# Optimization experiments

Measured on AMD Instinct MI355X. Metric: run time of the kernel, lower is better.

The kernel has to match this reference:

```python
import jax, jax.numpy as jnp
import numpy as np

N, E = 40000, 640000
IN, HID, OUT = 128, 128, 128


def _lin(key, fan_in, fan_out):
    bound = 1.0 / np.sqrt(fan_in)
    kw, kb = jax.random.split(key)
    W = jax.random.uniform(kw, (fan_in, fan_out), jnp.float32, -bound, bound)
    b = jax.random.uniform(kb, (fan_out,), jnp.float32, -bound, bound)
    return W, b


def setup_inputs() -> dict:
    key = jax.random.key(0)
    ks = jax.random.split(key, 10)
    node_feat = jax.random.normal(ks[0], (N, IN), jnp.float32)
    coord_feat = jax.random.normal(ks[1], (N, 3), jnp.float32)
    src = jax.random.randint(ks[2], (E,), 0, N, jnp.int32)
    dst = jax.random.randint(ks[3], (E,), 0, N, jnp.int32)
    # edge_mlp: Linear(2*IN+1 -> HID), SiLU, Linear(HID -> HID), SiLU
    We1, be1 = _lin(ks[4], 2 * IN + 1, HID)
    We2, be2 = _lin(ks[5], HID, HID)
    # node_mlp: Linear(IN+HID -> HID), SiLU, Linear(HID -> OUT)
    Wn1, bn1 = _lin(ks[6], IN + HID, HID)
    Wn2, bn2 = _lin(ks[7], HID, OUT)
    # coord_mlp: Linear(HID -> HID), SiLU, Linear(HID -> 1, bias=False)
    Wc1, bc1 = _lin(ks[8], HID, HID)
    Wc2, _ = _lin(ks[9], HID, 1)
    return {"node_feat": node_feat, "coord_feat": coord_feat, "src": src, "dst": dst,
            "We1": We1, "be1": be1, "We2": We2, "be2": be2,
            "Wn1": Wn1, "bn1": bn1, "Wn2": Wn2, "bn2": bn2,
            "Wc1": Wc1, "bc1": bc1, "Wc2": Wc2}


def reference(node_feat, coord_feat, src, dst,
              We1, be1, We2, be2, Wn1, bn1, Wn2, bn2, Wc1, bc1, Wc2):
    n = node_feat.shape[0]
    # edge gather: u_sub_v gives x_src - x_dst
    x_diff = coord_feat[src] - coord_feat[dst]                       # (E, 3)
    dist = jnp.sqrt(jnp.sum(x_diff * x_diff, axis=-1, keepdims=True))  # (E, 1)
    x_dir = x_diff / (dist + 1e-7)
    f = jnp.concatenate([node_feat[src], node_feat[dst], dist], axis=-1)  # (E, 2*IN+1)
    msg_h = jax.nn.silu(jax.nn.silu(f @ We1 + be1) @ We2 + be2)      # (E, HID)
    coef = jax.nn.silu(msg_h @ Wc1 + bc1) @ Wc2                      # (E, 1)
    msg_x = coef * x_dir                                             # (E, 3)
    # scatter-reduce to destination nodes: sum for h, mean for x
    h_neigh = jax.ops.segment_sum(msg_h, dst, num_segments=n)        # (N, HID)
    cnt = jax.ops.segment_sum(jnp.ones((dst.shape[0], 1), msg_x.dtype), dst, num_segments=n)
    x_neigh = jax.ops.segment_sum(msg_x, dst, num_segments=n) / jnp.maximum(cnt, 1.0)
    h = jax.nn.silu(jnp.concatenate([node_feat, h_neigh], axis=-1) @ Wn1 + bn1) @ Wn2 + bn2
    return h, coord_feat + x_neigh
```

## Files before the change

kernel.cpp:

```cpp
#include <hip/hip_runtime.h>
#include <hip/hip_bf16.h>
#include <math.h>
#include <stdint.h>

#define N_NODES 40000
#define N_EDGES 640000

typedef short short8 __attribute__((ext_vector_type(8)));
typedef float f32x4 __attribute__((ext_vector_type(4)));

__device__ __forceinline__ float silu(float x) {
    return __fdividef(x, 1.0f + __expf(-x));
}

__device__ __forceinline__ unsigned short f2bf(float f) {
    unsigned u = __float_as_uint(f);
    u += 0x7FFF + ((u >> 16) & 1);
    return (unsigned short)(u >> 16);
}
__device__ __forceinline__ float bf2f(unsigned short h) {
    return __uint_as_float(((unsigned)h) << 16);
}
__device__ __forceinline__ unsigned pk2bf(float a, float b) {
    __hip_bfloat162 h = __float22bfloat162_rn(make_float2(a, b));
    unsigned u;
    __builtin_memcpy(&u, &h, 4);
    return u;
}

__global__ __launch_bounds__(1024) void k_scan(const int* __restrict__ deg,
                                               int* __restrict__ row_start) {
    __shared__ int wsum[16];
    const int t = threadIdx.x;
    const int lane = t & 63, wid = t >> 6;
    int base = 0;
    if (t == 0) row_start[0] = 0;
    for (int off = 0; off < N_NODES; off += 1024) {
        int x = (off + t < N_NODES) ? deg[off + t] : 0;
#pragma unroll
        for (int s = 1; s < 64; s <<= 1) {
            const int u = __shfl_up(x, s, 64);
            if (lane >= s) x += u;
        }
        if (lane == 63) wsum[wid] = x;
        __syncthreads();
        if (wid == 0) {
            int ws = (lane < 16) ? wsum[lane] : 0;
#pragma unroll
            for (int s = 1; s < 16; s <<= 1) {
                const int u = __shfl_up(ws, s, 64);
                if (lane >= s) ws += u;
            }
            if (lane < 16) wsum[lane] = ws;
        }
        __syncthreads();
        const int wbase = (wid > 0) ? wsum[wid - 1] : 0;
        const int total = wsum[15];
        if (off + t < N_NODES) row_start[off + t + 1] = base + wbase + x;
        base += total;
        __syncthreads();
    }
}

__global__ __launch_bounds__(256) void k_fill(const int* __restrict__ dst,
                                              const int* __restrict__ row_start,
                                              int* __restrict__ cursor,
                                              int* __restrict__ elist) {
    const int e = blockIdx.x * 256 + threadIdx.x;
    if (e < N_EDGES) {
        const int d = dst[e];
        const int p = atomicAdd(&cursor[d], 1);
        elist[row_start[d] + p] = e;
    }
}

__global__ __launch_bounds__(128) void k_pack2(
    const float* __restrict__ We1, const float* __restrict__ We2,
    const float* __restrict__ Wc1, const float* __restrict__ Wn1,
    const float* __restrict__ Wn2,
    unsigned short* __restrict__ Wt_e1, unsigned short* __restrict__ Wt_e2,
    unsigned short* __restrict__ Wt_c1, unsigned short* __restrict__ Wt_n1,
    unsigned short* __restrict__ Wt_n2,
    int* __restrict__ deg, int* __restrict__ cursor, float* __restrict__ xs,
    float* __restrict__ hn) {
    const int b = blockIdx.x;
    const int t = threadIdx.x;
    Wt_e1[b * 128 + t] = f2bf(We1[(size_t)((b >> 7) * 128 + t) * 128 + (b & 127)]);
    if (b < 128) {
        Wt_e2[b * 128 + t] = f2bf(We2[(size_t)t * 128 + b]);
        Wt_c1[b * 128 + t] = f2bf(Wc1[(size_t)t * 128 + b]);
        Wt_n2[b * 128 + t] = f2bf(Wn2[(size_t)t * 128 + b]);
        Wt_n1[b * 256 + t] = f2bf(Wn1[(size_t)t * 128 + b]);
        Wt_n1[b * 256 + 128 + t] = f2bf(Wn1[(size_t)(128 + t) * 128 + b]);
    }
    const int gid = b * 128 + t;
    for (int i = gid; i < N_NODES; i += 32768) { deg[i] = 0; cursor[i] = 0; }
    for (int i = gid; i < N_NODES * 4; i += 32768) xs[i] = 0.0f;
    float4* hz = (float4*)hn;
    const float4 z4 = {0.f, 0.f, 0.f, 0.f};
    for (int i = gid; i < N_NODES * 32; i += 32768) hz[i] = z4;
}

__global__ __launch_bounds__(256) void k_cntpre(
    const float* __restrict__ nf, const unsigned short* __restrict__ Wt_e1,
    unsigned short* __restrict__ Pc,
    const int* __restrict__ dst, int* __restrict__ deg) {
    __shared__ __align__(16) unsigned short sNF[32][136];
    const int t = threadIdx.x;
    const int node0 = blockIdx.x * 32;
    {
        const int e0 = (blockIdx.x * 256 + t) * 2;
        const int d0 = dst[e0], d1 = dst[e0 + 1];
        atomicAdd(&deg[d0], 1);
        atomicAdd(&deg[d1], 1);
    }
    {
        const int m = t >> 3, kc = (t & 7) * 16;
        const float* sp = &nf[(size_t)(node0 + m) * 128 + kc];
        const float4 v0 = *(const float4*)(sp + 0);
        const float4 v1 = *(const float4*)(sp + 4);
        const float4 v2 = *(const float4*)(sp + 8);
        const float4 v3 = *(const float4*)(sp + 12);
        int4 o0, o1;
        o0.x = pk2bf(v0.x, v0.y); o0.y = pk2bf(v0.z, v0.w);
        o0.z = pk2bf(v1.x, v1.y); o0.w = pk2bf(v1.z, v1.w);
        o1.x = pk2bf(v2.x, v2.y); o1.y = pk2bf(v2.z, v2.w);
        o1.z = pk2bf(v3.x, v3.y); o1.w = pk2bf(v3.z, v3.w);
        *(int4*)&sNF[m][kc] = o0;
        *(int4*)&sNF[m][kc + 8] = o1;
    }
    __syncthreads();

    const int w = t >> 6, l = t & 63, c = l & 15, quad = l >> 4;
    const int n0 = w * 64;

    f32x4 acc[2][4];
#pragma unroll
    for (int mt = 0; mt < 2; mt++)
#pragma unroll
        for (int tile = 0; tile < 4; tile++) acc[mt][tile] = (f32x4){0.f, 0.f, 0.f, 0.f};

#pragma unroll
    for (int k0 = 0; k0 < 128; k0 += 32) {
        const short8 a0 = *(const short8*)&sNF[c][k0 + quad * 8];
        const short8 a1 = *(const short8*)&sNF[16 + c][k0 + quad * 8];
#pragma unroll
        for (int tile = 0; tile < 4; tile++) {
            const short8 b = *(const short8*)(Wt_e1 +
                ((size_t)(n0 + tile * 16 + c) << 7) + k0 + quad * 8);
            acc[0][tile] = __builtin_amdgcn_mfma_f32_16x16x32_bf16(a0, b, acc[0][tile], 0, 0, 0);
            acc[1][tile] = __builtin_amdgcn_mfma_f32_16x16x32_bf16(a1, b, acc[1][tile], 0, 0, 0);
        }
    }
#pragma unroll
    for (int mt = 0; mt < 2; mt++)
#pragma unroll
        for (int tile = 0; tile < 4; tile++) {
            const int col = n0 + tile * 16 + c;
            const unsigned p01 = pk2bf(acc[mt][tile][0], acc[mt][tile][1]);
            const unsigned p23 = pk2bf(acc[mt][tile][2], acc[mt][tile][3]);
            const int row = node0 + mt * 16 + quad * 4;
            Pc[(size_t)(row + 0) * 256 + col] = (unsigned short)p01;
            Pc[(size_t)(row + 1) * 256 + col] = (unsigned short)(p01 >> 16);
            Pc[(size_t)(row + 2) * 256 + col] = (unsigned short)p23;
            Pc[(size_t)(row + 3) * 256 + col] = (unsigned short)(p23 >> 16);
        }
}

__global__ __launch_bounds__(512) void k_edge5(
    const unsigned short* __restrict__ Pc, const float* __restrict__ coord,
    const int* __restrict__ src, const int* __restrict__ dst,
    const int* __restrict__ elist,
    const float* __restrict__ We1, const float* __restrict__ be1,
    const unsigned short* __restrict__ Wt_e2, const float* __restrict__ be2,
    const unsigned short* __restrict__ Wt_c1, const float* __restrict__ bc1,
    const float* __restrict__ Wc2,
    float* __restrict__ h_neigh, float* __restrict__ xs) {
    __shared__ __align__(16) unsigned short sT[128][136];
    __shared__ float scoefp[8][32];
    __shared__ float sw[128], sb[128];
    __shared__ float sdist[128];
    __shared__ float sxd[128][3];
    __shared__ int ssrc[128];
    __shared__ int sdst[128];

    const int t = threadIdx.x;
    const int e0 = blockIdx.x * 128;

    if (t < 128) {
        const int eid = elist[e0 + t];
        const int s = src[eid], d = dst[eid];
        ssrc[t] = s; sdst[t] = d;
        const float dx = coord[3 * s + 0] - coord[3 * d + 0];
        const float dy = coord[3 * s + 1] - coord[3 * d + 1];
        const float dz = coord[3 * s + 2] - coord[3 * d + 2];
        const float dist = sqrtf(dx * dx + dy * dy + dz * dz);
        sdist[t] = dist;
        const float inv = __fdividef(1.0f, dist + 1e-7f);
        sxd[t][0] = dx * inv; sxd[t][1] = dy * inv; sxd[t][2] = dz * inv;
    } else if (t < 160) {
        ((float4*)sw)[t - 128] = ((const float4*)(We1 + 256 * 128))[t - 128];
    } else if (t < 192) {
        ((float4*)sb)[t - 160] = ((const float4*)be1)[t - 160];
    }
    __syncthreads();

    {
        const int e = t >> 2;
        const int kc = (t & 3) * 32;
        const int s = ssrc[e], d = sdst[e];
        const float dist = sdist[e];
        const unsigned short* p1 = Pc + (size_t)s * 256 + kc;
        const unsigned short* p2 = Pc + (size_t)d * 256 + 128 + kc;
        short8 a[4], b[4];
#pragma unroll
        for (int i = 0; i < 4; i++) {
            a[i] = *(const short8*)(p1 + i * 8);
            b[i] = *(const short8*)(p2 + i * 8);
        }
#pragma unroll
        for (int i = 0; i < 4; i++) {
            float v[8];
#pragma unroll
            for (int kk = 0; kk < 8; kk++) {
                const int k = kc + i * 8 + kk;
                v[kk] = silu(bf2f((unsigned short)a[i][kk]) + bf2f((unsigned short)b[i][kk])
                             + dist * sw[k] + sb[k]);
            }
            int4 o;
            o.x = pk2bf(v[0], v[1]); o.y = pk2bf(v[2], v[3]);
            o.z = pk2bf(v[4], v[5]); o.w = pk2bf(v[6], v[7]);
            *(int4*)&sT[e][kc + i * 8] = o;
        }
    }
    __syncthreads();

    const int w = t >> 6;
    const int l = t & 63;
    const int h = w & 3;
    const int H = w >> 2;
    const int m0 = h * 32;
    const int n0 = H * 64;
    const int c = l & 15;
    const int quad = l >> 4;

    f32x4 acc1[2][4];
#pragma unroll
    for (int mt = 0; mt < 2; mt++)
#pragma unroll
        for (int tile = 0; tile < 4; tile++) acc1[mt][tile] = (f32x4){0.f, 0.f, 0.f, 0.f};
#pragma unroll
    for (int k0 = 0; k0 < 128; k0 += 32) {
        const short8 a0 = *(const short8*)&sT[m0 + c][k0 + quad * 8];
        const short8 a1 = *(const short8*)&sT[m0 + 16 + c][k0 + quad * 8];
#pragma unroll
        for (int tile = 0; tile < 4; tile++) {
            const short8 b = *(const short8*)(Wt_e2 +
                ((size_t)(n0 + tile * 16 + c) << 7) + k0 + quad * 8);
            acc1[0][tile] = __builtin_amdgcn_mfma_f32_16x16x32_bf16(a0, b, acc1[0][tile], 0, 0, 0);
            acc1[1][tile] = __builtin_amdgcn_mfma_f32_16x16x32_bf16(a1, b, acc1[1][tile], 0, 0, 0);
        }
    }
    __syncthreads();

#pragma unroll
    for (int mt = 0; mt < 2; mt++)
#pragma unroll
        for (int tile = 0; tile < 4; tile++) {
            const int col = n0 + tile * 16 + c;
            const float bb = be2[col];
            const unsigned p01 = pk2bf(silu(acc1[mt][tile][0] + bb), silu(acc1[mt][tile][1] + bb));
            const unsigned p23 = pk2bf(silu(acc1[mt][tile][2] + bb), silu(acc1[mt][tile][3] + bb));
            const int row = m0 + mt * 16 + quad * 4;
            sT[row + 0][col] = (unsigned short)p01;
            sT[row + 1][col] = (unsigned short)(p01 >> 16);
            sT[row + 2][col] = (unsigned short)p23;
            sT[row + 3][col] = (unsigned short)(p23 >> 16);
        }
    __syncthreads();

    {
        const int j = t & 127;
        const int q = t >> 7;
        const int eb = q * 32;
        float acc = bf2f(sT[eb][j]);
        int prev = sdst[eb];
        for (int e2 = eb + 1; e2 < eb + 32; e2++) {
            const int de = sdst[e2];
            if (de != prev) {
                atomicAdd(&h_neigh[(size_t)prev * 128 + j], acc);
                acc = 0.0f;
                prev = de;
            }
            acc += bf2f(sT[e2][j]);
        }
        atomicAdd(&h_neigh[(size_t)prev * 128 + j], acc);
    }

    {
        f32x4 acc[2][4];
#pragma unroll
        for (int mt = 0; mt < 2; mt++)
#pragma unroll
            for (int tile = 0; tile < 4; tile++) acc[mt][tile] = (f32x4){0.f, 0.f, 0.f, 0.f};
#pragma unroll
        for (int k0 = 0; k0 < 128; k0 += 32) {
            const short8 a0 = *(const short8*)&sT[m0 + c][k0 + quad * 8];
            const short8 a1 = *(const short8*)&sT[m0 + 16 + c][k0 + quad * 8];
#pragma unroll
            for (int tile = 0; tile < 4; tile++) {
                const short8 b = *(const short8*)(Wt_c1 +
                    ((size_t)(n0 + tile * 16 + c) << 7) + k0 + quad * 8);
                acc[0][tile] = __builtin_amdgcn_mfma_f32_16x16x32_bf16(a0, b, acc[0][tile], 0, 0, 0);
                acc[1][tile] = __builtin_amdgcn_mfma_f32_16x16x32_bf16(a1, b, acc[1][tile], 0, 0, 0);
            }
        }
        float part[2][4] = {{0.f, 0.f, 0.f, 0.f}, {0.f, 0.f, 0.f, 0.f}};
#pragma unroll
        for (int tile = 0; tile < 4; tile++) {
            const int col = n0 + tile * 16 + c;
            const float bc = bc1[col];
            const float wc = Wc2[col];
#pragma unroll
            for (int mt = 0; mt < 2; mt++)
#pragma unroll
                for (int r = 0; r < 4; r++)
                    part[mt][r] += silu(acc[mt][tile][r] + bc) * wc;
        }
#pragma unroll
        for (int off = 1; off < 16; off <<= 1) {
#pragma unroll
            for (int mt = 0; mt < 2; mt++)
#pragma unroll
                for (int r = 0; r < 4; r++)
                    part[mt][r] += __shfl_xor(part[mt][r], off, 64);
        }
        if (c == 0) {
#pragma unroll
            for (int mt = 0; mt < 2; mt++)
#pragma unroll
                for (int r = 0; r < 4; r++)
                    scoefp[w][mt * 16 + quad * 4 + r] = part[mt][r];
        }
    }

    if (l < 3) {
        const int cc = l;
        const int eb = h * 32;
        float acc = scoefp[w][0] * sxd[eb][cc];
        int prev = sdst[eb];
        for (int e2 = eb + 1; e2 < eb + 32; e2++) {
            const int de = sdst[e2];
            if (de != prev) {
                atomicAdd(&xs[(size_t)prev * 4 + cc], acc);
                acc = 0.0f;
                prev = de;
            }
            acc += scoefp[w][e2 & 31] * sxd[e2][cc];
        }
        atomicAdd(&xs[(size_t)prev * 4 + cc], acc);
    }
}

__global__ __launch_bounds__(256) void k_node(
    const float* __restrict__ nf, const float* __restrict__ coord,
    const float* __restrict__ hn, const float* __restrict__ xs,
    const int* __restrict__ row_start,
    const unsigned short* __restrict__ Wt_n1, const float* __restrict__ bn1,
    const unsigned short* __restrict__ Wt_n2, const float* __restrict__ bn2,
    float* __restrict__ out_h, float* __restrict__ out_x) {
    __shared__ __align__(16) unsigned short sAB[32][264];
    __shared__ __align__(16) unsigned short sH[32][136];
    const int t = threadIdx.x;
    const int node0 = blockIdx.x * 32;
    {
        const int m = t >> 3, kc = (t & 7) * 32;
        const float* base = (kc < 128) ? &nf[(size_t)(node0 + m) * 128 + kc]
                                       : &hn[(size_t)(node0 + m) * 128 + (kc - 128)];
#pragma unroll
        for (int kk = 0; kk < 32; kk += 8) {
            const float4 v0 = *(const float4*)(base + kk);
            const float4 v1 = *(const float4*)(base + kk + 4);
            int4 o;
            o.x = pk2bf(v0.x, v0.y); o.y = pk2bf(v0.z, v0.w);
            o.z = pk2bf(v1.x, v1.y); o.w = pk2bf(v1.z, v1.w);
            *(int4*)&sAB[m][kc + kk] = o;
        }
    }
    if (t < 96) {
        const int m = t / 3, cc = t - m * 3;
        const int i = node0 + m;
        const float cnt = (float)(row_start[i + 1] - row_start[i]);
        out_x[(size_t)i * 3 + cc] =
            coord[(size_t)i * 3 + cc] + __fdividef(xs[(size_t)i * 4 + cc], fmaxf(cnt, 1.0f));
    }
    __syncthreads();

    const int w = t >> 6, l = t & 63, c = l & 15, quad = l >> 4;
    const int n0 = w * 32;

    {
        f32x4 acc[2][2];
#pragma unroll
        for (int mt = 0; mt < 2; mt++)
#pragma unroll
            for (int tile = 0; tile < 2; tile++) acc[mt][tile] = (f32x4){0.f, 0.f, 0.f, 0.f};
#pragma unroll
        for (int k0 = 0; k0 < 256; k0 += 32) {
            const short8 a0 = *(const short8*)&sAB[c][k0 + quad * 8];
            const short8 a1 = *(const short8*)&sAB[16 + c][k0 + quad * 8];
#pragma unroll
            for (int tile = 0; tile < 2; tile++) {
                const short8 b = *(const short8*)(Wt_n1 +
                    ((size_t)(n0 + tile * 16 + c) << 8) + k0 + quad * 8);
                acc[0][tile] = __builtin_amdgcn_mfma_f32_16x16x32_bf16(a0, b, acc[0][tile], 0, 0, 0);
                acc[1][tile] = __builtin_amdgcn_mfma_f32_16x16x32_bf16(a1, b, acc[1][tile], 0, 0, 0);
            }
        }
#pragma unroll
        for (int mt = 0; mt < 2; mt++)
#pragma unroll
            for (int tile = 0; tile < 2; tile++) {
                const int col = n0 + tile * 16 + c;
                const float bb = bn1[col];
                const unsigned p01 = pk2bf(silu(acc[mt][tile][0] + bb), silu(acc[mt][tile][1] + bb));
                const unsigned p23 = pk2bf(silu(acc[mt][tile][2] + bb), silu(acc[mt][tile][3] + bb));
                const int row = mt * 16 + quad * 4;
                sH[row + 0][col] = (unsigned short)p01;
                sH[row + 1][col] = (unsigned short)(p01 >> 16);
                sH[row + 2][col] = (unsigned short)p23;
                sH[row + 3][col] = (unsigned short)(p23 >> 16);
            }
    }
    __syncthreads();

    {
        f32x4 acc[2][2];
#pragma unroll
        for (int mt = 0; mt < 2; mt++)
#pragma unroll
            for (int tile = 0; tile < 2; tile++) acc[mt][tile] = (f32x4){0.f, 0.f, 0.f, 0.f};
#pragma unroll
        for (int k0 = 0; k0 < 128; k0 += 32) {
            const short8 a0 = *(const short8*)&sH[c][k0 + quad * 8];
            const short8 a1 = *(const short8*)&sH[16 + c][k0 + quad * 8];
#pragma unroll
            for (int tile = 0; tile < 2; tile++) {
                const short8 b = *(const short8*)(Wt_n2 +
                    ((size_t)(n0 + tile * 16 + c) << 7) + k0 + quad * 8);
                acc[0][tile] = __builtin_amdgcn_mfma_f32_16x16x32_bf16(a0, b, acc[0][tile], 0, 0, 0);
                acc[1][tile] = __builtin_amdgcn_mfma_f32_16x16x32_bf16(a1, b, acc[1][tile], 0, 0, 0);
            }
        }
#pragma unroll
        for (int mt = 0; mt < 2; mt++)
#pragma unroll
            for (int tile = 0; tile < 2; tile++) {
                const int col = n0 + tile * 16 + c;
                const float bb = bn2[col];
#pragma unroll
                for (int r = 0; r < 4; r++) {
                    const int row = mt * 16 + quad * 4 + r;
                    out_h[(size_t)(node0 + row) * 128 + col] = acc[mt][tile][r] + bb;
                }
            }
    }
}

extern "C" void kernel_launch(void* const* d_in, const int* in_sizes, int n_in,
                              void* d_out, int out_size, void* d_ws, size_t ws_size,
                              hipStream_t stream) {
    const float* nf    = (const float*)d_in[0];
    const float* coord = (const float*)d_in[1];
    const int*   src   = (const int*)d_in[2];
    const int*   dst   = (const int*)d_in[3];
    const float* We1   = (const float*)d_in[4];
    const float* be1   = (const float*)d_in[5];
    const float* We2   = (const float*)d_in[6];
    const float* be2   = (const float*)d_in[7];
    const float* Wn1   = (const float*)d_in[8];
    const float* bn1   = (const float*)d_in[9];
    const float* Wn2   = (const float*)d_in[10];
    const float* bn2   = (const float*)d_in[11];
    const float* Wc1   = (const float*)d_in[12];
    const float* bc1   = (const float*)d_in[13];
    const float* Wc2   = (const float*)d_in[14];

    unsigned short* Pc = (unsigned short*)d_ws;
    float* hn = (float*)(Pc + (size_t)N_NODES * 256);
    float* xs = hn + (size_t)N_NODES * 128;
    int* deg       = (int*)(xs + (size_t)N_NODES * 4);
    int* row_start = deg + N_NODES;
    int* cursor    = row_start + N_NODES + 1;
    int* elist     = cursor + N_NODES;
    unsigned short* Wt_e1 = (unsigned short*)
        (((uintptr_t)(elist + N_EDGES) + 255) & ~(uintptr_t)255);
    unsigned short* Wt_e2 = Wt_e1 + 256 * 128;
    unsigned short* Wt_c1 = Wt_e2 + 128 * 128;
    unsigned short* Wt_n1 = Wt_c1 + 128 * 128;
    unsigned short* Wt_n2 = Wt_n1 + 128 * 256;

    float* out_h = (float*)d_out;
    float* out_x = out_h + (size_t)N_NODES * 128;

    k_pack2<<<256, 128, 0, stream>>>(We1, We2, Wc1, Wn1, Wn2,
                                     Wt_e1, Wt_e2, Wt_c1, Wt_n1, Wt_n2,
                                     deg, cursor, xs, hn);
    k_cntpre<<<N_NODES / 32, 256, 0, stream>>>(nf, Wt_e1, Pc, dst, deg);
    k_scan<<<1, 1024, 0, stream>>>(deg, row_start);
    k_fill<<<(N_EDGES + 255) / 256, 256, 0, stream>>>(dst, row_start, cursor, elist);
    k_edge5<<<N_EDGES / 128, 512, 0, stream>>>(Pc, coord, src, dst, elist,
                                               We1, be1, Wt_e2, be2, Wt_c1, bc1,
                                               Wc2, hn, xs);
    k_node<<<N_NODES / 32, 256, 0, stream>>>(nf, coord, hn, xs, row_start,
                                             Wt_n1, bn1, Wt_n2, bn2, out_h, out_x);
}
```

Measured before the change: 476.6 us.

## Restructure edge kernel into per-wave 16-edge tiles with no block barriers

The edge kernel now gives each wave its own independent 16-edge tile, with 256-thread blocks and launch bounds of 8. After the initial load, the MLP stages sync only within the wave (lgkmcnt waits) instead of with block-wide barriers. The be1 bias is folded into the precomputed Pc table, and a block-index swizzle spreads CSR-sorted edge ranges across the grid. MFMA loops are wrapped in s_setprio. The aim is to remove barrier stalls, cut LDS use so more waves fit per CU, and overlap the irregular gathers. In exchange, each Wt_e2/Wt_c1 fragment serves only 16 edges instead of 32, so there is more weight traffic per edge and more segmented atomics at the smaller tile boundaries.

```diff
diff --git a/kernel.cpp b/kernel.cpp
--- a/kernel.cpp
+++ b/kernel.cpp
@@ -103,6 +103,7 @@
 
 __global__ __launch_bounds__(256) void k_cntpre(
     const float* __restrict__ nf, const unsigned short* __restrict__ Wt_e1,
+    const float* __restrict__ be1,
     unsigned short* __restrict__ Pc,
     const int* __restrict__ dst, int* __restrict__ deg) {
     __shared__ __align__(16) unsigned short sNF[32][136];
@@ -157,8 +158,9 @@
 #pragma unroll
         for (int tile = 0; tile < 4; tile++) {
             const int col = n0 + tile * 16 + c;
-            const unsigned p01 = pk2bf(acc[mt][tile][0], acc[mt][tile][1]);
-            const unsigned p23 = pk2bf(acc[mt][tile][2], acc[mt][tile][3]);
+            const float bias = (col >= 128) ? be1[col - 128] : 0.0f;
+            const unsigned p01 = pk2bf(acc[mt][tile][0] + bias, acc[mt][tile][1] + bias);
+            const unsigned p23 = pk2bf(acc[mt][tile][2] + bias, acc[mt][tile][3] + bias);
             const int row = node0 + mt * 16 + quad * 4;
             Pc[(size_t)(row + 0) * 256 + col] = (unsigned short)p01;
             Pc[(size_t)(row + 1) * 256 + col] = (unsigned short)(p01 >> 16);
@@ -167,49 +169,50 @@
         }
 }
 
-__global__ __launch_bounds__(512) void k_edge5(
+__global__ __launch_bounds__(256, 8) void k_edge6(
     const unsigned short* __restrict__ Pc, const float* __restrict__ coord,
     const int* __restrict__ src, const int* __restrict__ dst,
     const int* __restrict__ elist,
-    const float* __restrict__ We1, const float* __restrict__ be1,
+    const float* __restrict__ We1,
     const unsigned short* __restrict__ Wt_e2, const float* __restrict__ be2,
     const unsigned short* __restrict__ Wt_c1, const float* __restrict__ bc1,
     const float* __restrict__ Wc2,
     float* __restrict__ h_neigh, float* __restrict__ xs) {
-    __shared__ __align__(16) unsigned short sT[128][136];
-    __shared__ float scoefp[8][32];
-    __shared__ float sw[128], sb[128];
-    __shared__ float sdist[128];
-    __shared__ float sxd[128][3];
-    __shared__ int ssrc[128];
-    __shared__ int sdst[128];
+    __shared__ __align__(16) unsigned short sT[4][16][136];
+    __shared__ float sw[128];
+    __shared__ float sdist[4][16];
+    __shared__ float sxd[4][16][3];
+    __shared__ int ssrc[4][16];
+    __shared__ int sdst[4][16];
+    __shared__ float scoef[4][16];
 
     const int t = threadIdx.x;
-    const int e0 = blockIdx.x * 128;
-
-    if (t < 128) {
-        const int eid = elist[e0 + t];
+    const int w = t >> 6, l = t & 63;
+
+    const int bid = (int)blockIdx.x;
+    const int swz = (bid & 7) * 1250 + (bid >> 3);
+    const int e0 = swz * 64 + w * 16;
+
+    if (l < 16) {
+        const int eid = elist[e0 + l];
         const int s = src[eid], d = dst[eid];
-        ssrc[t] = s; sdst[t] = d;
+        ssrc[w][l] = s; sdst[w][l] = d;
         const float dx = coord[3 * s + 0] - coord[3 * d + 0];
         const float dy = coord[3 * s + 1] - coord[3 * d + 1];
         const float dz = coord[3 * s + 2] - coord[3 * d + 2];
         const float dist = sqrtf(dx * dx + dy * dy + dz * dz);
-        sdist[t] = dist;
+        sdist[w][l] = dist;
         const float inv = __fdividef(1.0f, dist + 1e-7f);
-        sxd[t][0] = dx * inv; sxd[t][1] = dy * inv; sxd[t][2] = dz * inv;
-    } else if (t < 160) {
-        ((float4*)sw)[t - 128] = ((const float4*)(We1 + 256 * 128))[t - 128];
-    } else if (t < 192) {
-        ((float4*)sb)[t - 160] = ((const float4*)be1)[t - 160];
-    }
+        sxd[w][l][0] = dx * inv; sxd[w][l][1] = dy * inv; sxd[w][l][2] = dz * inv;
+    }
+    if (t < 32) ((float4*)sw)[t] = ((const float4*)(We1 + 256 * 128))[t];
     __syncthreads();
 
     {
-        const int e = t >> 2;
-        const int kc = (t & 3) * 32;
-        const int s = ssrc[e], d = sdst[e];
-        const float dist = sdist[e];
+        const int e = l >> 2;
+        const int kc = (l & 3) * 32;
+        const int s = ssrc[w][e], d = sdst[w][e];
+        const float dist = sdist[w][e];
         const unsigned short* p1 = Pc + (size_t)s * 256 + kc;
         const unsigned short* p2 = Pc + (size_t)d * 256 + 128 + kc;
         short8 a[4], b[4];
@@ -225,138 +228,134 @@
             for (int kk = 0; kk < 8; kk++) {
                 const int k = kc + i * 8 + kk;
                 v[kk] = silu(bf2f((unsigned short)a[i][kk]) + bf2f((unsigned short)b[i][kk])
-                             + dist * sw[k] + sb[k]);
+                             + dist * sw[k]);
             }
             int4 o;
             o.x = pk2bf(v[0], v[1]); o.y = pk2bf(v[2], v[3]);
             o.z = pk2bf(v[4], v[5]); o.w = pk2bf(v[6], v[7]);
-            *(int4*)&sT[e][kc + i * 8] = o;
-        }
-    }
-    __syncthreads();
-
-    const int w = t >> 6;
-    const int l = t & 63;
-    const int h = w & 3;
-    const int H = w >> 2;
-    const int m0 = h * 32;
-    const int n0 = H * 64;
-    const int c = l & 15;
-    const int quad = l >> 4;
-
-    f32x4 acc1[2][4];
-#pragma unroll
-    for (int mt = 0; mt < 2; mt++)
-#pragma unroll
-        for (int tile = 0; tile < 4; tile++) acc1[mt][tile] = (f32x4){0.f, 0.f, 0.f, 0.f};
-#pragma unroll
-    for (int k0 = 0; k0 < 128; k0 += 32) {
-        const short8 a0 = *(const short8*)&sT[m0 + c][k0 + quad * 8];
-        const short8 a1 = *(const short8*)&sT[m0 + 16 + c][k0 + quad * 8];
+            *(int4*)&sT[w][e][kc + i * 8] = o;
+        }
+    }
+    asm volatile("s_waitcnt lgkmcnt(0)" ::: "memory");
+
+    const int c = l & 15, quad = l >> 4;
+
+    short8 aQ[4];
+#pragma unroll
+    for (int k0 = 0; k0 < 4; k0++)
+        aQ[k0] = *(const short8*)&sT[w][c][k0 * 32 + quad * 8];
+
+#pragma unroll
+    for (int nh = 0; nh < 2; nh++) {
+        f32x4 acc[4];
+#pragma unroll
+        for (int tile = 0; tile < 4; tile++) acc[tile] = (f32x4){0.f, 0.f, 0.f, 0.f};
+        __builtin_amdgcn_s_setprio(1);
+#pragma unroll
+        for (int k0 = 0; k0 < 4; k0++) {
+#pragma unroll
+            for (int tile = 0; tile < 4; tile++) {
+                const short8 b = *(const short8*)(Wt_e2 +
+                    ((size_t)(nh * 64 + tile * 16 + c) << 7) + k0 * 32 + quad * 8);
+                acc[tile] = __builtin_amdgcn_mfma_f32_16x16x32_bf16(aQ[k0], b, acc[tile], 0, 0, 0);
+            }
+        }
+        __builtin_amdgcn_s_setprio(0);
 #pragma unroll
         for (int tile = 0; tile < 4; tile++) {
-            const short8 b = *(const short8*)(Wt_e2 +
-                ((size_t)(n0 + tile * 16 + c) << 7) + k0 + quad * 8);
-            acc1[0][tile] = __builtin_amdgcn_mfma_f32_16x16x32_bf16(a0, b, acc1[0][tile], 0, 0, 0);
-            acc1[1][tile] = __builtin_amdgcn_mfma_f32_16x16x32_bf16(a1, b, acc1[1][tile], 0, 0, 0);
-        }
-    }
-    __syncthreads();
-
-#pragma unroll
-    for (int mt = 0; mt < 2; mt++)
-#pragma unroll
-        for (int tile = 0; tile < 4; tile++) {
-            const int col = n0 + tile * 16 + c;
+            const int col = nh * 64 + tile * 16 + c;
             const float bb = be2[col];
-            const unsigned p01 = pk2bf(silu(acc1[mt][tile][0] + bb), silu(acc1[mt][tile][1] + bb));
-            const unsigned p23 = pk2bf(silu(acc1[mt][tile][2] + bb), silu(acc1[mt][tile][3] + bb));
-            const int row = m0 + mt * 16 + quad * 4;
-            sT[row + 0][col] = (unsigned short)p01;
-            sT[row + 1][col] = (unsigned short)(p01 >> 16);
-            sT[row + 2][col] = (unsigned short)p23;
-            sT[row + 3][col] = (unsigned short)(p23 >> 16);
-        }
-    __syncthreads();
-
-    {
-        const int j = t & 127;
-        const int q = t >> 7;
-        const int eb = q * 32;
-        float acc = bf2f(sT[eb][j]);
-        int prev = sdst[eb];
-        for (int e2 = eb + 1; e2 < eb + 32; e2++) {
-            const int de = sdst[e2];
+            const unsigned p01 = pk2bf(silu(acc[tile][0] + bb), silu(acc[tile][1] + bb));
+            const unsigned p23 = pk2bf(silu(acc[tile][2] + bb), silu(acc[tile][3] + bb));
+            const int row = quad * 4;
+            sT[w][row + 0][col] = (unsigned short)p01;
+            sT[w][row + 1][col] = (unsigned short)(p01 >> 16);
+            sT[w][row + 2][col] = (unsigned short)p23;
+            sT[w][row + 3][col] = (unsigned short)(p23 >> 16);
+        }
+    }
+    asm volatile("s_waitcnt lgkmcnt(0)" ::: "memory");
+
+    short8 aQ2[4];
+#pragma unroll
+    for (int k0 = 0; k0 < 4; k0++)
+        aQ2[k0] = *(const short8*)&sT[w][c][k0 * 32 + quad * 8];
+
+    {
+        float a0 = bf2f(sT[w][0][l]);
+        float a1 = bf2f(sT[w][0][64 + l]);
+        int prev = sdst[w][0];
+#pragma unroll
+        for (int e2 = 1; e2 < 16; e2++) {
+            const int de = sdst[w][e2];
             if (de != prev) {
-                atomicAdd(&h_neigh[(size_t)prev * 128 + j], acc);
-                acc = 0.0f;
+                atomicAdd(&h_neigh[(size_t)prev * 128 + l], a0);
+                atomicAdd(&h_neigh[(size_t)prev * 128 + 64 + l], a1);
+                a0 = 0.0f; a1 = 0.0f;
                 prev = de;
             }
-            acc += bf2f(sT[e2][j]);
-        }
-        atomicAdd(&h_neigh[(size_t)prev * 128 + j], acc);
-    }
-
-    {
-        f32x4 acc[2][4];
-#pragma unroll
-        for (int mt = 0; mt < 2; mt++)
-#pragma unroll
-            for (int tile = 0; tile < 4; tile++) acc[mt][tile] = (f32x4){0.f, 0.f, 0.f, 0.f};
-#pragma unroll
-        for (int k0 = 0; k0 < 128; k0 += 32) {
-            const short8 a0 = *(const short8*)&sT[m0 + c][k0 + quad * 8];
-            const short8 a1 = *(const short8*)&sT[m0 + 16 + c][k0 + quad * 8];
+            a0 += bf2f(sT[w][e2][l]);
+            a1 += bf2f(sT[w][e2][64 + l]);
+        }
+        atomicAdd(&h_neigh[(size_t)prev * 128 + l], a0);
+        atomicAdd(&h_neigh[(size_t)prev * 128 + 64 + l], a1);
+    }
+
+    {
+        float part[4] = {0.f, 0.f, 0.f, 0.f};
+#pragma unroll
+        for (int nh = 0; nh < 2; nh++) {
+            f32x4 acc[4];
+#pragma unroll
+            for (int tile = 0; tile < 4; tile++) acc[tile] = (f32x4){0.f, 0.f, 0.f, 0.f};
+            __builtin_amdgcn_s_setprio(1);
+#pragma unroll
+            for (int k0 = 0; k0 < 4; k0++) {
+#pragma unroll
+                for (int tile = 0; tile < 4; tile++) {
+                    const short8 b = *(const short8*)(Wt_c1 +
+                        ((size_t)(nh * 64 + tile * 16 + c) << 7) + k0 * 32 + quad * 8);
+                    acc[tile] = __builtin_amdgcn_mfma_f32_16x16x32_bf16(aQ2[k0], b, acc[tile], 0, 0, 0);
+                }
+            }
+            __builtin_amdgcn_s_setprio(0);
 #pragma unroll
             for (int tile = 0; tile < 4; tile++) {
-                const short8 b = *(const short8*)(Wt_c1 +
-                    ((size_t)(n0 + tile * 16 + c) << 7) + k0 + quad * 8);
-                acc[0][tile] = __builtin_amdgcn_mfma_f32_16x16x32_bf16(a0, b, acc[0][tile], 0, 0, 0);
-                acc[1][tile] = __builtin_amdgcn_mfma_f32_16x16x32_bf16(a1, b, acc[1][tile], 0, 0, 0);
-            }
-        }
-        float part[2][4] = {{0.f, 0.f, 0.f, 0.f}, {0.f, 0.f, 0.f, 0.f}};
-#pragma unroll
-        for (int tile = 0; tile < 4; tile++) {
-            const int col = n0 + tile * 16 + c;
-            const float bc = bc1[col];
-            const float wc = Wc2[col];
-#pragma unroll
-            for (int mt = 0; mt < 2; mt++)
+                const int col = nh * 64 + tile * 16 + c;
+                const float bc = bc1[col];
+                const float wc = Wc2[col];
 #pragma unroll
                 for (int r = 0; r < 4; r++)
-                    part[mt][r] += silu(acc[mt][tile][r] + bc) * wc;
+                    part[r] += silu(acc[tile][r] + bc) * wc;
+            }
         }
 #pragma unroll
         for (int off = 1; off < 16; off <<= 1) {
 #pragma unroll
-            for (int mt = 0; mt < 2; mt++)
-#pragma unroll
-                for (int r = 0; r < 4; r++)
-                    part[mt][r] += __shfl_xor(part[mt][r], off, 64);
+            for (int r = 0; r < 4; r++)
+                part[r] += __shfl_xor(part[r], off, 64);
         }
         if (c == 0) {
 #pragma unroll
-            for (int mt = 0; mt < 2; mt++)
-#pragma unroll
-                for (int r = 0; r < 4; r++)
-                    scoefp[w][mt * 16 + quad * 4 + r] = part[mt][r];
-        }
-    }
+            for (int r = 0; r < 4; r++)
+                scoef[w][quad * 4 + r] = part[r];
+        }
+    }
+    asm volatile("s_waitcnt lgkmcnt(0)" ::: "memory");
 
     if (l < 3) {
         const int cc = l;
-        const int eb = h * 32;
-        float acc = scoefp[w][0] * sxd[eb][cc];
-        int prev = sdst[eb];
-        for (int e2 = eb + 1; e2 < eb + 32; e2++) {
-            const int de = sdst[e2];
+        float acc = scoef[w][0] * sxd[w][0][cc];
+        int prev = sdst[w][0];
+#pragma unroll
+        for (int e2 = 1; e2 < 16; e2++) {
+            const int de = sdst[w][e2];
             if (de != prev) {
                 atomicAdd(&xs[(size_t)prev * 4 + cc], acc);
                 acc = 0.0f;
                 prev = de;
             }
-            acc += scoefp[w][e2 & 31] * sxd[e2][cc];
+            acc += scoef[w][e2] * sxd[w][e2][cc];
         }
         atomicAdd(&xs[(size_t)prev * 4 + cc], acc);
     }
@@ -506,12 +505,12 @@
     k_pack2<<<256, 128, 0, stream>>>(We1, We2, Wc1, Wn1, Wn2,
                                      Wt_e1, Wt_e2, Wt_c1, Wt_n1, Wt_n2,
                                      deg, cursor, xs, hn);
-    k_cntpre<<<N_NODES / 32, 256, 0, stream>>>(nf, Wt_e1, Pc, dst, deg);
+    k_cntpre<<<N_NODES / 32, 256, 0, stream>>>(nf, Wt_e1, be1, Pc, dst, deg);
     k_scan<<<1, 1024, 0, stream>>>(deg, row_start);
     k_fill<<<(N_EDGES + 255) / 256, 256, 0, stream>>>(dst, row_start, cursor, elist);
-    k_edge5<<<N_EDGES / 128, 512, 0, stream>>>(Pc, coord, src, dst, elist,
-                                               We1, be1, Wt_e2, be2, Wt_c1, bc1,
-                                               Wc2, hn, xs);
+    k_edge6<<<N_EDGES / 64, 256, 0, stream>>>(Pc, coord, src, dst, elist,
+                                              We1, Wt_e2, be2, Wt_c1, bc1,
+                                              Wc2, hn, xs);
     k_node<<<N_NODES / 32, 256, 0, stream>>>(nf, coord, hn, xs, row_start,
                                              Wt_n1, bn1, Wt_n2, bn2, out_h, out_x);
 }
```

Measured after the change: 613.1 us. 28.6% more time.

## Process four edge tiles per block with software-pipelined gather prefetch

Applied to the files above, without the earlier changes.

The edge kernel now processes 512 edges per block as four 128-edge tiles. It double-buffers the per-edge metadata and prefetches the next tile's elist, src/dst, coords and Pc gathers while the current tile runs its MFMA and scatter work. The be1 bias is folded into the precomputed Pc projection, so the edge kernel no longer adds it per element. A block-index swizzle remaps blocks to contiguous edge ranges per XCD, and launch bounds request 4 blocks per CU. Each iteration adds extra barriers and register pressure from the prefetched gathers, and the bias is now added before bf16 rounding of Pc.

```diff
diff --git a/kernel.cpp b/kernel.cpp
--- a/kernel.cpp
+++ b/kernel.cpp
@@ -103,6 +103,7 @@
 
 __global__ __launch_bounds__(256) void k_cntpre(
     const float* __restrict__ nf, const unsigned short* __restrict__ Wt_e1,
+    const float* __restrict__ be1,
     unsigned short* __restrict__ Pc,
     const int* __restrict__ dst, int* __restrict__ deg) {
     __shared__ __align__(16) unsigned short sNF[32][136];
@@ -157,8 +158,9 @@
 #pragma unroll
         for (int tile = 0; tile < 4; tile++) {
             const int col = n0 + tile * 16 + c;
-            const unsigned p01 = pk2bf(acc[mt][tile][0], acc[mt][tile][1]);
-            const unsigned p23 = pk2bf(acc[mt][tile][2], acc[mt][tile][3]);
+            const float bias = (col >= 128) ? be1[col - 128] : 0.0f;
+            const unsigned p01 = pk2bf(acc[mt][tile][0] + bias, acc[mt][tile][1] + bias);
+            const unsigned p23 = pk2bf(acc[mt][tile][2] + bias, acc[mt][tile][3] + bias);
             const int row = node0 + mt * 16 + quad * 4;
             Pc[(size_t)(row + 0) * 256 + col] = (unsigned short)p01;
             Pc[(size_t)(row + 1) * 256 + col] = (unsigned short)(p01 >> 16);
@@ -167,198 +169,232 @@
         }
 }
 
-__global__ __launch_bounds__(512) void k_edge5(
+__global__ __launch_bounds__(512, 4) void k_edge7(
     const unsigned short* __restrict__ Pc, const float* __restrict__ coord,
     const int* __restrict__ src, const int* __restrict__ dst,
-    const int* __restrict__ elist,
-    const float* __restrict__ We1, const float* __restrict__ be1,
+    const int* __restrict__ elist, const float* __restrict__ We1,
     const unsigned short* __restrict__ Wt_e2, const float* __restrict__ be2,
     const unsigned short* __restrict__ Wt_c1, const float* __restrict__ bc1,
     const float* __restrict__ Wc2,
     float* __restrict__ h_neigh, float* __restrict__ xs) {
     __shared__ __align__(16) unsigned short sT[128][136];
+    __shared__ float sw[128];
     __shared__ float scoefp[8][32];
-    __shared__ float sw[128], sb[128];
-    __shared__ float sdist[128];
-    __shared__ float sxd[128][3];
-    __shared__ int ssrc[128];
-    __shared__ int sdst[128];
+    __shared__ int ssrc[2][128], sdst[2][128];
+    __shared__ float sdist[2][128];
+    __shared__ float sxd[2][128][3];
 
     const int t = threadIdx.x;
-    const int e0 = blockIdx.x * 128;
+    const int w = t >> 6, l = t & 63;
+    const int h = w & 3, H = w >> 2;
+    const int m0 = h * 32, n0 = H * 64;
+    const int c = l & 15, quad = l >> 4;
+
+    const int bid = (int)blockIdx.x;
+    const int xcd = bid & 7, jj = bid >> 3;
+    const int swz = (xcd < 2 ? xcd * 157 : 314 + (xcd - 2) * 156) + jj;
+    const int ebase = swz * 512;
 
     if (t < 128) {
-        const int eid = elist[e0 + t];
+        const int eid = elist[ebase + t];
         const int s = src[eid], d = dst[eid];
-        ssrc[t] = s; sdst[t] = d;
+        ssrc[0][t] = s; sdst[0][t] = d;
         const float dx = coord[3 * s + 0] - coord[3 * d + 0];
         const float dy = coord[3 * s + 1] - coord[3 * d + 1];
         const float dz = coord[3 * s + 2] - coord[3 * d + 2];
         const float dist = sqrtf(dx * dx + dy * dy + dz * dz);
-        sdist[t] = dist;
+        sdist[0][t] = dist;
         const float inv = __fdividef(1.0f, dist + 1e-7f);
-        sxd[t][0] = dx * inv; sxd[t][1] = dy * inv; sxd[t][2] = dz * inv;
+        sxd[0][t][0] = dx * inv; sxd[0][t][1] = dy * inv; sxd[0][t][2] = dz * inv;
     } else if (t < 160) {
         ((float4*)sw)[t - 128] = ((const float4*)(We1 + 256 * 128))[t - 128];
-    } else if (t < 192) {
-        ((float4*)sb)[t - 160] = ((const float4*)be1)[t - 160];
     }
     __syncthreads();
 
+    short8 ga[4], gb[4];
     {
-        const int e = t >> 2;
-        const int kc = (t & 3) * 32;
-        const int s = ssrc[e], d = sdst[e];
-        const float dist = sdist[e];
-        const unsigned short* p1 = Pc + (size_t)s * 256 + kc;
-        const unsigned short* p2 = Pc + (size_t)d * 256 + 128 + kc;
-        short8 a[4], b[4];
+        const int e_ = t >> 2, kc_ = (t & 3) * 32;
+        const int s_ = ssrc[0][e_], d_ = sdst[0][e_];
+        const unsigned short* p1 = Pc + (size_t)s_ * 256 + kc_;
+        const unsigned short* p2 = Pc + (size_t)d_ * 256 + 128 + kc_;
 #pragma unroll
         for (int i = 0; i < 4; i++) {
-            a[i] = *(const short8*)(p1 + i * 8);
-            b[i] = *(const short8*)(p2 + i * 8);
-        }
-#pragma unroll
-        for (int i = 0; i < 4; i++) {
-            float v[8];
-#pragma unroll
-            for (int kk = 0; kk < 8; kk++) {
-                const int k = kc + i * 8 + kk;
-                v[kk] = silu(bf2f((unsigned short)a[i][kk]) + bf2f((unsigned short)b[i][kk])
-                             + dist * sw[k] + sb[k]);
-            }
-            int4 o;
-            o.x = pk2bf(v[0], v[1]); o.y = pk2bf(v[2], v[3]);
-            o.z = pk2bf(v[4], v[5]); o.w = pk2bf(v[6], v[7]);
-            *(int4*)&sT[e][kc + i * 8] = o;
-        }
-    }
-    __syncthreads();
-
-    const int w = t >> 6;
-    const int l = t & 63;
-    const int h = w & 3;
-    const int H = w >> 2;
-    const int m0 = h * 32;
-    const int n0 = H * 64;
-    const int c = l & 15;
-    const int quad = l >> 4;
-
-    f32x4 acc1[2][4];
-#pragma unroll
-    for (int mt = 0; mt < 2; mt++)
-#pragma unroll
-        for (int tile = 0; tile < 4; tile++) acc1[mt][tile] = (f32x4){0.f, 0.f, 0.f, 0.f};
-#pragma unroll
-    for (int k0 = 0; k0 < 128; k0 += 32) {
-        const short8 a0 = *(const short8*)&sT[m0 + c][k0 + quad * 8];
-        const short8 a1 = *(const short8*)&sT[m0 + 16 + c][k0 + quad * 8];
-#pragma unroll
-        for (int tile = 0; tile < 4; tile++) {
-            const short8 b = *(const short8*)(Wt_e2 +
-                ((size_t)(n0 + tile * 16 + c) << 7) + k0 + quad * 8);
-            acc1[0][tile] = __builtin_amdgcn_mfma_f32_16x16x32_bf16(a0, b, acc1[0][tile], 0, 0, 0);
-            acc1[1][tile] = __builtin_amdgcn_mfma_f32_16x16x32_bf16(a1, b, acc1[1][tile], 0, 0, 0);
-        }
-    }
-    __syncthreads();
-
-#pragma unroll
-    for (int mt = 0; mt < 2; mt++)
-#pragma unroll
-        for (int tile = 0; tile < 4; tile++) {
-            const int col = n0 + tile * 16 + c;
-            const float bb = be2[col];
-            const unsigned p01 = pk2bf(silu(acc1[mt][tile][0] + bb), silu(acc1[mt][tile][1] + bb));
-            const unsigned p23 = pk2bf(silu(acc1[mt][tile][2] + bb), silu(acc1[mt][tile][3] + bb));
-            const int row = m0 + mt * 16 + quad * 4;
-            sT[row + 0][col] = (unsigned short)p01;
-            sT[row + 1][col] = (unsigned short)(p01 >> 16);
-            sT[row + 2][col] = (unsigned short)p23;
-            sT[row + 3][col] = (unsigned short)(p23 >> 16);
-        }
-    __syncthreads();
-
-    {
-        const int j = t & 127;
-        const int q = t >> 7;
-        const int eb = q * 32;
-        float acc = bf2f(sT[eb][j]);
-        int prev = sdst[eb];
-        for (int e2 = eb + 1; e2 < eb + 32; e2++) {
-            const int de = sdst[e2];
-            if (de != prev) {
-                atomicAdd(&h_neigh[(size_t)prev * 128 + j], acc);
-                acc = 0.0f;
-                prev = de;
-            }
-            acc += bf2f(sT[e2][j]);
-        }
-        atomicAdd(&h_neigh[(size_t)prev * 128 + j], acc);
-    }
-
-    {
-        f32x4 acc[2][4];
+            ga[i] = *(const short8*)(p1 + i * 8);
+            gb[i] = *(const short8*)(p2 + i * 8);
+        }
+    }
+
+    int eid_n = 0, s_n = 0, d_n = 0;
+
+    for (int ti = 0; ti < 4; ++ti) {
+        const int CUR = ti & 1;
+        const int NXT = CUR ^ 1;
+        const bool DO_PF = (ti < 3);
+        if (ti) __syncthreads();
+
+        {
+            const int e = t >> 2, kc = (t & 3) * 32;
+            const float dist = sdist[CUR][e];
+#pragma unroll
+            for (int i = 0; i < 4; i++) {
+                float v[8];
+#pragma unroll
+                for (int kk = 0; kk < 8; kk++) {
+                    const int k = kc + i * 8 + kk;
+                    v[kk] = silu(bf2f((unsigned short)ga[i][kk]) +
+                                 bf2f((unsigned short)gb[i][kk]) + dist * sw[k]);
+                }
+                int4 o;
+                o.x = pk2bf(v[0], v[1]); o.y = pk2bf(v[2], v[3]);
+                o.z = pk2bf(v[4], v[5]); o.w = pk2bf(v[6], v[7]);
+                *(int4*)&sT[e][kc + i * 8] = o;
+            }
+        }
+        if (DO_PF && t < 128) eid_n = elist[ebase + (ti + 1) * 128 + t];
+        __syncthreads();
+
+        f32x4 acc1[2][4];
 #pragma unroll
         for (int mt = 0; mt < 2; mt++)
 #pragma unroll
-            for (int tile = 0; tile < 4; tile++) acc[mt][tile] = (f32x4){0.f, 0.f, 0.f, 0.f};
+            for (int tile = 0; tile < 4; tile++) acc1[mt][tile] = (f32x4){0.f, 0.f, 0.f, 0.f};
 #pragma unroll
         for (int k0 = 0; k0 < 128; k0 += 32) {
             const short8 a0 = *(const short8*)&sT[m0 + c][k0 + quad * 8];
             const short8 a1 = *(const short8*)&sT[m0 + 16 + c][k0 + quad * 8];
 #pragma unroll
             for (int tile = 0; tile < 4; tile++) {
-                const short8 b = *(const short8*)(Wt_c1 +
+                const short8 b = *(const short8*)(Wt_e2 +
                     ((size_t)(n0 + tile * 16 + c) << 7) + k0 + quad * 8);
-                acc[0][tile] = __builtin_amdgcn_mfma_f32_16x16x32_bf16(a0, b, acc[0][tile], 0, 0, 0);
-                acc[1][tile] = __builtin_amdgcn_mfma_f32_16x16x32_bf16(a1, b, acc[1][tile], 0, 0, 0);
-            }
-        }
-        float part[2][4] = {{0.f, 0.f, 0.f, 0.f}, {0.f, 0.f, 0.f, 0.f}};
-#pragma unroll
-        for (int tile = 0; tile < 4; tile++) {
-            const int col = n0 + tile * 16 + c;
-            const float bc = bc1[col];
-            const float wc = Wc2[col];
+                acc1[0][tile] = __builtin_amdgcn_mfma_f32_16x16x32_bf16(a0, b, acc1[0][tile], 0, 0, 0);
+                acc1[1][tile] = __builtin_amdgcn_mfma_f32_16x16x32_bf16(a1, b, acc1[1][tile], 0, 0, 0);
+            }
+        }
+        if (DO_PF && t < 128) { s_n = src[eid_n]; d_n = dst[eid_n]; }
+        __syncthreads();
+
+        float cdx = 0.f, cdy = 0.f, cdz = 0.f;
+        if (DO_PF && t < 128) {
+            cdx = coord[3 * s_n + 0] - coord[3 * d_n + 0];
+            cdy = coord[3 * s_n + 1] - coord[3 * d_n + 1];
+            cdz = coord[3 * s_n + 2] - coord[3 * d_n + 2];
+        }
+#pragma unroll
+        for (int mt = 0; mt < 2; mt++)
+#pragma unroll
+            for (int tile = 0; tile < 4; tile++) {
+                const int col = n0 + tile * 16 + c;
+                const float bb = be2[col];
+                const unsigned p01 = pk2bf(silu(acc1[mt][tile][0] + bb), silu(acc1[mt][tile][1] + bb));
+                const unsigned p23 = pk2bf(silu(acc1[mt][tile][2] + bb), silu(acc1[mt][tile][3] + bb));
+                const int row = m0 + mt * 16 + quad * 4;
+                sT[row + 0][col] = (unsigned short)p01;
+                sT[row + 1][col] = (unsigned short)(p01 >> 16);
+                sT[row + 2][col] = (unsigned short)p23;
+                sT[row + 3][col] = (unsigned short)(p23 >> 16);
+            }
+        if (DO_PF && t < 128) {
+            ssrc[NXT][t] = s_n; sdst[NXT][t] = d_n;
+            const float dist = sqrtf(cdx * cdx + cdy * cdy + cdz * cdz);
+            sdist[NXT][t] = dist;
+            const float inv = __fdividef(1.0f, dist + 1e-7f);
+            sxd[NXT][t][0] = cdx * inv; sxd[NXT][t][1] = cdy * inv; sxd[NXT][t][2] = cdz * inv;
+        }
+        __syncthreads();
+
+        if (DO_PF) {
+            const int e_ = t >> 2, kc_ = (t & 3) * 32;
+            const int s_ = ssrc[NXT][e_], d_ = sdst[NXT][e_];
+            const unsigned short* p1 = Pc + (size_t)s_ * 256 + kc_;
+            const unsigned short* p2 = Pc + (size_t)d_ * 256 + 128 + kc_;
+#pragma unroll
+            for (int i = 0; i < 4; i++) {
+                ga[i] = *(const short8*)(p1 + i * 8);
+                gb[i] = *(const short8*)(p2 + i * 8);
+            }
+        }
+
+        {
+            const int j = t & 127;
+            const int q = t >> 7;
+            const int eb = q * 32;
+            float acc = bf2f(sT[eb][j]);
+            int prev = sdst[CUR][eb];
+            for (int e2 = eb + 1; e2 < eb + 32; e2++) {
+                const int de = sdst[CUR][e2];
+                if (de != prev) {
+                    atomicAdd(&h_neigh[(size_t)prev * 128 + j], acc);
+                    acc = 0.0f;
+                    prev = de;
+                }
+                acc += bf2f(sT[e2][j]);
+            }
+            atomicAdd(&h_neigh[(size_t)prev * 128 + j], acc);
+        }
+
+        {
+            f32x4 acc[2][4];
 #pragma unroll
             for (int mt = 0; mt < 2; mt++)
 #pragma unroll
-                for (int r = 0; r < 4; r++)
-                    part[mt][r] += silu(acc[mt][tile][r] + bc) * wc;
-        }
-#pragma unroll
-        for (int off = 1; off < 16; off <<= 1) {
-#pragma unroll
-            for (int mt = 0; mt < 2; mt++)
-#pragma unroll
-                for (int r = 0; r < 4; r++)
-                    part[mt][r] += __shfl_xor(part[mt][r], off, 64);
-        }
-        if (c == 0) {
-#pragma unroll
-            for (int mt = 0; mt < 2; mt++)
-#pragma unroll
-                for (int r = 0; r < 4; r++)
-                    scoefp[w][mt * 16 + quad * 4 + r] = part[mt][r];
-        }
-    }
-
-    if (l < 3) {
-        const int cc = l;
-        const int eb = h * 32;
-        float acc = scoefp[w][0] * sxd[eb][cc];
-        int prev = sdst[eb];
-        for (int e2 = eb + 1; e2 < eb + 32; e2++) {
-            const int de = sdst[e2];
-            if (de != prev) {
-                atomicAdd(&xs[(size_t)prev * 4 + cc], acc);
-                acc = 0.0f;
-                prev = de;
-            }
-            acc += scoefp[w][e2 & 31] * sxd[e2][cc];
-        }
-        atomicAdd(&xs[(size_t)prev * 4 + cc], acc);
+                for (int tile = 0; tile < 4; tile++) acc[mt][tile] = (f32x4){0.f, 0.f, 0.f, 0.f};
+#pragma unroll
+            for (int k0 = 0; k0 < 128; k0 += 32) {
+                const short8 a0 = *(const short8*)&sT[m0 + c][k0 + quad * 8];
+                const short8 a1 = *(const short8*)&sT[m0 + 16 + c][k0 + quad * 8];
+#pragma unroll
+                for (int tile = 0; tile < 4; tile++) {
+                    const short8 b = *(const short8*)(Wt_c1 +
+                        ((size_t)(n0 + tile * 16 + c) << 7) + k0 + quad * 8);
+                    acc[0][tile] = __builtin_amdgcn_mfma_f32_16x16x32_bf16(a0, b, acc[0][tile], 0, 0, 0);
+                    acc[1][tile] = __builtin_amdgcn_mfma_f32_16x16x32_bf16(a1, b, acc[1][tile], 0, 0, 0);
+                }
+            }
+            float part[2][4] = {{0.f, 0.f, 0.f, 0.f}, {0.f, 0.f, 0.f, 0.f}};
+#pragma unroll
+            for (int tile = 0; tile < 4; tile++) {
+                const int col = n0 + tile * 16 + c;
+                const float bc = bc1[col];
+                const float wc = Wc2[col];
+#pragma unroll
+                for (int mt = 0; mt < 2; mt++)
+#pragma unroll
+                    for (int r = 0; r < 4; r++)
+                        part[mt][r] += silu(acc[mt][tile][r] + bc) * wc;
+            }
+#pragma unroll
+            for (int off = 1; off < 16; off <<= 1) {
+#pragma unroll
+                for (int mt = 0; mt < 2; mt++)
+#pragma unroll
+                    for (int r = 0; r < 4; r++)
+                        part[mt][r] += __shfl_xor(part[mt][r], off, 64);
+            }
+            if (c == 0) {
+#pragma unroll
+                for (int mt = 0; mt < 2; mt++)
+#pragma unroll
+                    for (int r = 0; r < 4; r++)
+                        scoefp[w][mt * 16 + quad * 4 + r] = part[mt][r];
+            }
+        }
+
+        if (l < 3) {
+            const int cc = l;
+            const int eb = h * 32;
+            float acc = scoefp[w][0] * sxd[CUR][eb][cc];
+            int prev = sdst[CUR][eb];
+            for (int e2 = eb + 1; e2 < eb + 32; e2++) {
+                const int de = sdst[CUR][e2];
+                if (de != prev) {
+                    atomicAdd(&xs[(size_t)prev * 4 + cc], acc);
+                    acc = 0.0f;
+                    prev = de;
+                }
+                acc += scoefp[w][e2 & 31] * sxd[CUR][e2][cc];
+            }
+            atomicAdd(&xs[(size_t)prev * 4 + cc], acc);
+        }
     }
 }
 
@@ -506,11 +542,11 @@
     k_pack2<<<256, 128, 0, stream>>>(We1, We2, Wc1, Wn1, Wn2,
                                      Wt_e1, Wt_e2, Wt_c1, Wt_n1, Wt_n2,
                                      deg, cursor, xs, hn);
-    k_cntpre<<<N_NODES / 32, 256, 0, stream>>>(nf, Wt_e1, Pc, dst, deg);
+    k_cntpre<<<N_NODES / 32, 256, 0, stream>>>(nf, Wt_e1, be1, Pc, dst, deg);
     k_scan<<<1, 1024, 0, stream>>>(deg, row_start);
     k_fill<<<(N_EDGES + 255) / 256, 256, 0, stream>>>(dst, row_start, cursor, elist);
-    k_edge5<<<N_EDGES / 128, 512, 0, stream>>>(Pc, coord, src, dst, elist,
-                                               We1, be1, Wt_e2, be2, Wt_c1, bc1,
+    k_edge7<<<N_EDGES / 512, 512, 0, stream>>>(Pc, coord, src, dst, elist,
+                                               We1, Wt_e2, be2, Wt_c1, bc1,
                                                Wc2, hn, xs);
     k_node<<<N_NODES / 32, 256, 0, stream>>>(nf, coord, hn, xs, row_start,
                                              Wt_n1, bn1, Wt_n2, bn2, out_h, out_x);
```

Result: slower. 674.2 us (+41.5%).
